# Kernel tuning notes

Measured on AMD Instinct MI355X. Metric: run time of the kernel, lower is better.

The kernel has to match this reference:

```python
import jax, jax.numpy as jnp
import numpy as np

EPS = 1e-5
NHEAD = 8
NEG = -1e9  # matches -inf masked-fill semantics; rows never fully masked after fallback


def layer_norm(x, g, b):
    m = jnp.mean(x, axis=-1, keepdims=True)
    v = jnp.var(x, axis=-1, keepdims=True)
    return (x - m) * jax.lax.rsqrt(v + EPS) * g + b


def mha(q, k, v, Wqkv, bqkv, Wo, bo, bias=None):
    # torch nn.MultiheadAttention math (batch_first). Wqkv: [C, 3C] (jax layout).
    B, N, C = q.shape
    M = k.shape[1]
    d = C // NHEAD
    Wq, Wk, Wv = jnp.split(Wqkv, 3, axis=1)
    bq, bk, bv = jnp.split(bqkv, 3)
    qp = (q @ Wq + bq).reshape(B, N, NHEAD, d)
    kp = (k @ Wk + bk).reshape(B, M, NHEAD, d)
    vp = (v @ Wv + bv).reshape(B, M, NHEAD, d)
    s = jnp.einsum('bnhd,bmhd->bhnm', qp, kp) / np.sqrt(d).astype(q.dtype)
    if bias is not None:
        s = s + bias  # [B,1,N,M] broadcast over heads
    a = jax.nn.softmax(s, axis=-1)
    o = jnp.einsum('bhnm,bmhd->bnhd', a, vp).reshape(B, N, C)
    return o @ Wo + bo


def setup_inputs() -> dict:
    key = jax.random.key(0)
    B, Nq, HW, C, F = 8, 100, 4096, 512, 2048
    ks = jax.random.split(key, 16)
    s = 0.02
    inp = {
        'q': jax.random.normal(ks[0], (B, Nq, C), jnp.float32),
        'kv': jax.random.normal(ks[1], (B, HW, C), jnp.float32),
        'mask_bin': jax.random.randint(ks[2], (B, Nq, HW), 0, 2, jnp.int32),
        # MaskedXAttn: attn params + norm_q/norm_kv
        'xa_Wqkv': jax.random.normal(ks[3], (C, 3 * C), jnp.float32) * s,
        'xa_bqkv': jnp.zeros((3 * C,), jnp.float32),
        'xa_Wo': jax.random.normal(ks[4], (C, C), jnp.float32) * s,
        'xa_bo': jnp.zeros((C,), jnp.float32),
        'xa_gq': jnp.ones((C,), jnp.float32),
        'xa_bq_ln': jnp.zeros((C,), jnp.float32),
        'xa_gkv': jnp.ones((C,), jnp.float32),
        'xa_bkv_ln': jnp.zeros((C,), jnp.float32),
        # self-attention
        'sa_Wqkv': jax.random.normal(ks[5], (C, 3 * C), jnp.float32) * s,
        'sa_bqkv': jnp.zeros((3 * C,), jnp.float32),
        'sa_Wo': jax.random.normal(ks[6], (C, C), jnp.float32) * s,
        'sa_bo': jnp.zeros((C,), jnp.float32),
        # norms
        'n1_g': jnp.ones((C,), jnp.float32), 'n1_b': jnp.zeros((C,), jnp.float32),
        'n2_g': jnp.ones((C,), jnp.float32), 'n2_b': jnp.zeros((C,), jnp.float32),
        # FFN (MLP with num_layers=2: Linear(C,F), ReLU, Linear(F,C))
        'ff_W1': jax.random.normal(ks[7], (C, F), jnp.float32) * s,
        'ff_b1': jnp.zeros((F,), jnp.float32),
        'ff_W2': jax.random.normal(ks[8], (F, C), jnp.float32) * s,
        'ff_b2': jnp.zeros((C,), jnp.float32),
    }
    return inp


def reference(q, kv, mask_bin,
              xa_Wqkv, xa_bqkv, xa_Wo, xa_bo, xa_gq, xa_bq_ln, xa_gkv, xa_bkv_ln,
              sa_Wqkv, sa_bqkv, sa_Wo, sa_bo,
              n1_g, n1_b, n2_g, n2_b,
              ff_W1, ff_b1, ff_W2, ff_b2):
    # --- masked cross-attention (vectorized equivalent of per-query loop) ---
    qn = layer_norm(q, xa_gq, xa_bq_ln)
    kvn = layer_norm(kv, xa_gkv, xa_bkv_ln)
    allow = mask_bin.astype(bool)                      # [B,Nq,HW] True = attend
    row_any = jnp.any(allow, axis=-1, keepdims=True)   # queries with empty mask -> full attention
    eff = jnp.where(row_any, allow, True)
    bias = jnp.where(eff, 0.0, NEG).astype(q.dtype)[:, None, :, :]  # [B,1,Nq,HW]
    xa = mha(qn, kvn, kvn, xa_Wqkv, xa_bqkv, xa_Wo, xa_bo, bias=bias)
    q = q + xa
    # --- self-attention over queries ---
    qn1 = layer_norm(q, n1_g, n1_b)
    sa = mha(qn1, qn1, qn1, sa_Wqkv, sa_bqkv, sa_Wo, sa_bo)
    q = q + sa
    # --- FFN ---
    qn2 = layer_norm(q, n2_g, n2_b)
    h = jax.nn.relu(qn2 @ ff_W1 + ff_b1)
    q = q + (h @ ff_W2 + ff_b2)
    return q
```

## Files before the change

### kernel.cpp

```cpp
#include <hip/hip_runtime.h>

typedef unsigned short u16;
typedef unsigned int u32;
typedef __bf16 bf16x8 __attribute__((ext_vector_type(8)));
typedef short s16x4 __attribute__((ext_vector_type(4)));
typedef float f32x4 __attribute__((ext_vector_type(4)));

#define NEG_INF -3.0e38f
#define QSCALE 0.18033688011f

__device__ __forceinline__ u16 f2bf(float f){
  union { float f; u32 u; } v; v.f = f;
  u32 r = v.u + 0x7fffu + ((v.u >> 16) & 1u);
  return (u16)(r >> 16);
}
__device__ __forceinline__ float bf2f(u16 h){
  union { u32 u; float f; } v; v.u = ((u32)h) << 16; return v.f;
}
__device__ __forceinline__ short f2bf_s(float f){
  union { __bf16 h; short s; } cv; cv.h = (__bf16)f; return cv.s;
}

__device__ __forceinline__ f32x4 mfma16(s16x4 a, s16x4 b, f32x4 c){
#if __has_builtin(__builtin_amdgcn_mfma_f32_16x16x16bf16_1k)
  return __builtin_amdgcn_mfma_f32_16x16x16bf16_1k(a, b, c, 0, 0, 0);
#else
  asm("v_mfma_f32_16x16x16_bf16 %0, %1, %2, %0" : "+v"(c) : "v"(a), "v"(b));
  return c;
#endif
}

__device__ __forceinline__ void gl_lds16(const void* g, void* l){
  __builtin_amdgcn_global_load_lds((const __attribute__((address_space(1))) void*)g,
      (__attribute__((address_space(3))) void*)l, 16, 0, 0);
}

__device__ __forceinline__ void ln_body(const float* __restrict__ xr,
    const float* __restrict__ g, const float* __restrict__ b,
    u16* __restrict__ orow, int lane){
  float4 v0 = *(const float4*)(xr + lane * 4);
  float4 v1 = *(const float4*)(xr + 256 + lane * 4);
  float s = v0.x+v0.y+v0.z+v0.w + v1.x+v1.y+v1.z+v1.w;
  float q = v0.x*v0.x+v0.y*v0.y+v0.z*v0.z+v0.w*v0.w
          + v1.x*v1.x+v1.y*v1.y+v1.z*v1.z+v1.w*v1.w;
  #pragma unroll
  for (int d=1; d<64; d<<=1){ s += __shfl_xor(s, d, 64); q += __shfl_xor(q, d, 64); }
  float mean = s * (1.0f/512.0f);
  float var  = q * (1.0f/512.0f) - mean*mean;
  float rs = rsqrtf(var + 1e-5f);
  float4 g0 = *(const float4*)(g + lane*4), g1 = *(const float4*)(g + 256 + lane*4);
  float4 b0 = *(const float4*)(b + lane*4), b1 = *(const float4*)(b + 256 + lane*4);
  uint2 pa, pb;
  pa.x = (u32)f2bf((v0.x-mean)*rs*g0.x + b0.x) | ((u32)f2bf((v0.y-mean)*rs*g0.y + b0.y) << 16);
  pa.y = (u32)f2bf((v0.z-mean)*rs*g0.z + b0.z) | ((u32)f2bf((v0.w-mean)*rs*g0.w + b0.w) << 16);
  pb.x = (u32)f2bf((v1.x-mean)*rs*g1.x + b1.x) | ((u32)f2bf((v1.y-mean)*rs*g1.y + b1.y) << 16);
  pb.y = (u32)f2bf((v1.z-mean)*rs*g1.z + b1.z) | ((u32)f2bf((v1.w-mean)*rs*g1.w + b1.w) << 16);
  *(uint2*)(orow + lane*4) = pa;
  *(uint2*)(orow + 256 + lane*4) = pb;
}

__global__ __launch_bounds__(256) void ln_rows(const float* __restrict__ x,
    const float* __restrict__ g, const float* __restrict__ b,
    u16* __restrict__ out, int rows){
  int wid = threadIdx.x >> 6, lane = threadIdx.x & 63;
  int row = blockIdx.x * 4 + wid;
  if (row >= rows) return;
  ln_body(x + (size_t)row*512, g, b, out + (size_t)row*512, lane);
}

struct WtJobs {
  const float* W[7]; u16* Wt[7];
  int K[7], Nfull[7], ncol0[7], nt[7], blk0[7];
};
struct PrepArgs {
  WtJobs wt; int totW;
  const float *x0, *g0, *b0; u16* o0; int nb0, rows0;
  const float *x1, *g1, *b1; u16* o1; int nb1, rows1;
};

__global__ __launch_bounds__(256) void prep_all(PrepArgs P){
  __shared__ float tile[32][33];
  int bb = blockIdx.x;
  int tid = threadIdx.x;
  int wid = tid >> 6, lane = tid & 63;
  if (bb < P.totW){
    const WtJobs& J = P.wt;
    const float* W = J.W[0]; u16* Wt = J.Wt[0];
    int K = J.K[0], Nfull = J.Nfull[0], ncol0 = J.ncol0[0], nt = J.nt[0], blk0 = 0;
    #pragma unroll
    for (int i=1;i<7;i++)
      if (bb >= J.blk0[i]){
        W=J.W[i]; Wt=J.Wt[i]; K=J.K[i]; Nfull=J.Nfull[i]; ncol0=J.ncol0[i]; nt=J.nt[i]; blk0=J.blk0[i];
      }
    int lb = bb - blk0;
    int tk = lb / nt, tn = lb % nt;
    int col = tid & 31, kr = tid >> 5;
    #pragma unroll
    for (int i=0;i<4;i++){
      int k = tk*32 + kr + i*8;
      tile[kr + i*8][col] = W[(size_t)k*Nfull + ncol0 + tn*32 + col];
    }
    __syncthreads();
    int nl = tid >> 3, kc = (tid & 7) * 4;
    uint2 o;
    o.x = (u32)f2bf(tile[kc+0][nl]) | ((u32)f2bf(tile[kc+1][nl]) << 16);
    o.y = (u32)f2bf(tile[kc+2][nl]) | ((u32)f2bf(tile[kc+3][nl]) << 16);
    *(uint2*)(Wt + (size_t)(tn*32 + nl)*K + tk*32 + kc) = o;
  } else if (bb < P.totW + P.nb0){
    int row = (bb - P.totW)*4 + wid;
    if (row >= P.rows0) return;
    ln_body(P.x0 + (size_t)row*512, P.g0, P.b0, P.o0 + (size_t)row*512, lane);
  } else {
    int row = (bb - P.totW - P.nb0)*4 + wid;
    if (row >= P.rows1) return;
    ln_body(P.x1 + (size_t)row*512, P.g1, P.b1, P.o1 + (size_t)row*512, lane);
  }
}

struct GemmJob {
  const u16* A; const u16* Bt; const float* bias;
  float* outf; u16* outb; const float* res; u16* out2;
  int M, N, K, lda, k0, ksplit, scale_cols, T1, rows_per_b, vstride, swz, brmap, blk0, nblk;
};
struct GemmJobs {
  GemmJob j[2]; int njobs;
  const int* mask; u32* mw; int maskBlk0;
};

template<int EPI>
__device__ __forceinline__ void epi_store(const GemmJob& J, f32x4 (&acc)[4][4],
    int m0, int n0, int wm, int wn, int lg, int l15, int ksp, u16* smem){
  if (EPI == 3){
    float bv[4];
    #pragma unroll
    for (int ni=0;ni<4;ni++) bv[ni] = J.bias[n0 + wn*64 + ni*16 + l15];
    if (n0 + 128 <= J.T1){
      #pragma unroll
      for (int ni=0;ni<4;ni++){
        int c = n0 + wn*64 + ni*16 + l15;
        #pragma unroll
        for (int mi=0;mi<4;mi++){
          int mr0 = m0 + wm*64 + mi*16 + lg*4;
          #pragma unroll
          for (int r4=0;r4<4;r4++)
            J.outb[(size_t)(mr0+r4)*J.T1 + c] = f2bf(acc[mi][ni][r4] + bv[ni]);
        }
      }
    } else {
      __syncthreads();
      char* scr = (char*)(smem + (wm*2 + wn)*4096);
      #pragma unroll
      for (int ni=0;ni<4;ni++){
        int f_loc = ni*16 + l15;
        #pragma unroll
        for (int mi=0;mi<4;mi++){
          int kb = mi*32 + lg*8;
          uint2 o;
          o.x = (u32)f2bf(acc[mi][ni][0]+bv[ni]) | ((u32)f2bf(acc[mi][ni][1]+bv[ni])<<16);
          o.y = (u32)f2bf(acc[mi][ni][2]+bv[ni]) | ((u32)f2bf(acc[mi][ni][3]+bv[ni])<<16);
          *(uint2*)(scr + f_loc*128 + (kb ^ ((f_loc&7)<<4))) = o;
        }
      }
      int lane = lg*16 + l15;
      int m_base = m0 + wm*64;
      int bidx = m_base >> 12;
      int key0 = m_base & 4095;
      int kc = lane & 7;
      #pragma unroll
      for (int it=0; it<8; it++){
        int f_loc = it*8 + (lane >> 3);
        uint4 v = *(const uint4*)(scr + f_loc*128 + ((kc<<4) ^ ((f_loc&7)<<4)));
        int fg = (n0 - J.T1) + wn*64 + f_loc;
        *(uint4*)(J.out2 + ((size_t)bidx*512 + fg)*(size_t)J.vstride + key0 + kc*8) = v;
      }
    }
  } else if (EPI == 4){
    #pragma unroll
    for (int mi=0;mi<4;mi++){
      #pragma unroll
      for (int r4=0;r4<4;r4++){
        int m = m0 + wm*64 + mi*16 + lg*4 + r4;
        if (m >= J.M) continue;
        float rb = J.bias[m];
        #pragma unroll
        for (int ni=0;ni<4;ni++){
          int c = n0 + wn*64 + ni*16 + l15;
          J.outb[(size_t)m*J.N + c] = f2bf(acc[mi][ni][r4] + rb);
        }
      }
    }
  } else if (EPI == 5){
    float* po_ = J.outf + (size_t)ksp*J.M*J.N;
    #pragma unroll
    for (int mi=0;mi<4;mi++){
      #pragma unroll
      for (int r4=0;r4<4;r4++){
        int m = m0 + wm*64 + mi*16 + lg*4 + r4;
        if (m >= J.M) continue;
        #pragma unroll
        for (int ni=0;ni<4;ni++){
          int c = n0 + wn*64 + ni*16 + l15;
          po_[(size_t)m*J.N + c] = acc[mi][ni][r4];
        }
      }
    }
  } else {
    float bv[4], scl[4];
    #pragma unroll
    for (int ni=0;ni<4;ni++){
      int c = n0 + wn*64 + ni*16 + l15;
      bv[ni]  = J.bias[c];
      scl[ni] = (c < J.scale_cols) ? QSCALE : 1.0f;
    }
    #pragma unroll
    for (int mi=0;mi<4;mi++){
      #pragma unroll
      for (int r4=0;r4<4;r4++){
        int m = m0 + wm*64 + mi*16 + lg*4 + r4;
        if (m >= J.M) continue;
        #pragma unroll
        for (int ni=0;ni<4;ni++){
          int c = n0 + wn*64 + ni*16 + l15;
          float v = acc[mi][ni][r4] + bv[ni];
          if (EPI == 0){
            J.outb[(size_t)m*J.N + c] = f2bf(v*scl[ni]);
          } else if (EPI == 1){
            J.outb[(size_t)m*J.N + c] = f2bf(fmaxf(v, 0.0f));
          } else {
            J.outf[(size_t)m*J.N + c] = v + J.res[(size_t)m*J.N + c];
          }
        }
      }
    }
  }
}

template<int EPI>
__device__ __forceinline__ void gemm_block(const GemmJob& J, int bidIn, u16* smem){
  u16* As = smem;
  u16* Bs = smem + 8192;
  int bid = bidIn;
  int ksp = 0;
  if (J.ksplit > 1){ ksp = bid / J.nblk; bid = bid % J.nblk; }
  if (J.swz){ int cpx = J.nblk >> 3; bid = (bid & 7)*cpx + (bid >> 3); }
  int NT = J.N >> 7;
  int mt = bid / NT, nt = bid % NT;
  int m0 = mt << 7, n0 = nt << 7;
  int kofs = J.k0 + ksp * J.K;
  int tid = threadIdx.x;
  int wid = tid >> 6, lane = tid & 63;
  int wm = wid >> 1, wn = wid & 1;
  int lg = lane >> 4, l15 = lane & 15;

  f32x4 acc[4][4] = {};
  int ktiles = J.K >> 6;
  for (int kt = 0; kt < ktiles; ++kt){
    int k0 = kofs + (kt << 6);
    if (kt) __syncthreads();
    #pragma unroll
    for (int i=0;i<4;i++){
      int L = i*4096 + tid*16;
      int T = L ^ (((L>>7)&7)<<4);
      int row = T >> 7, colb = T & 127;
      int ga = m0 + row; if (ga > J.M-1) ga = J.M-1;
      gl_lds16((const char*)J.A + ((size_t)ga*J.lda + k0)*2 + colb, (char*)As + L);
    }
    #pragma unroll
    for (int i=0;i<4;i++){
      int L = i*4096 + tid*16;
      int T = L ^ (((L>>7)&7)<<4);
      int row = T >> 7, colb = T & 127;
      int rowg = n0 + row;
      if (J.brmap){ int rb = rowg & 127; rowg = (rowg>>7)*J.brmap + (rb < J.brmap ? rb : J.brmap-1); }
      gl_lds16((const char*)J.Bt + ((size_t)rowg*J.lda + k0)*2 + colb, (char*)Bs + L);
    }
    __syncthreads();
    #pragma unroll
    for (int ks=0; ks<2; ++ks){
      bf16x8 af[4], bfr[4];
      #pragma unroll
      for (int mi=0; mi<4; ++mi){
        int r = wm*64 + mi*16 + l15;
        int byt = r*128 + ks*64 + lg*16;
        af[mi] = *(const bf16x8*)((const char*)As + (byt ^ ((r&7)<<4)));
      }
      #pragma unroll
      for (int ni=0; ni<4; ++ni){
        int r = wn*64 + ni*16 + l15;
        int byt = r*128 + ks*64 + lg*16;
        bfr[ni] = *(const bf16x8*)((const char*)Bs + (byt ^ ((r&7)<<4)));
      }
      __builtin_amdgcn_s_setprio(1);
      #pragma unroll
      for (int mi=0;mi<4;mi++)
        #pragma unroll
        for (int ni=0;ni<4;ni++)
          acc[mi][ni] = __builtin_amdgcn_mfma_f32_16x16x32_bf16(af[mi], bfr[ni], acc[mi][ni], 0,0,0);
      __builtin_amdgcn_s_setprio(0);
    }
  }
  epi_store<EPI>(J, acc, m0, n0, wm, wn, lg, l15, ksp, smem);
}

template<int EPIA, int EPIB>
__global__ __launch_bounds__(256) void gemm_multi(GemmJobs G){
  __shared__ __align__(16) u16 smem[16384];
  if (G.mask && (int)blockIdx.x >= G.maskBlk0){
    unsigned long long* blds = (unsigned long long*)smem;
    int tid = threadIdx.x;
    int wid = tid >> 6;
    int lb = (int)blockIdx.x - G.maskBlk0;
    int r0 = lb*2 + (wid >> 1);
    int word = tid & 127;
    const int* mr = G.mask + (size_t)r0*4096 + word*32;
    u32 w = 0;
    #pragma unroll
    for (int j=0;j<32;j+=4){
      int4 v = *(const int4*)(mr + j);
      w |= (u32)(v.x!=0) << j;
      w |= (u32)(v.y!=0) << (j+1);
      w |= (u32)(v.z!=0) << (j+2);
      w |= (u32)(v.w!=0) << (j+3);
    }
    blds[wid] = __ballot(w != 0);
    __syncthreads();
    bool any = (wid < 2) ? ((blds[0] | blds[1]) != 0ull) : ((blds[2] | blds[3]) != 0ull);
    G.mw[(size_t)r0*128 + word] = any ? w : 0xffffffffu;
    return;
  }
  bool second = (G.njobs > 1) && ((int)blockIdx.x >= G.j[1].blk0);
  if (second) gemm_block<EPIB>(G.j[1], (int)blockIdx.x - G.j[1].blk0, smem);
  else        gemm_block<EPIA>(G.j[0], (int)blockIdx.x, smem);
}

__global__ __launch_bounds__(256) void splitk_reduce(
    const float* __restrict__ part, int nsplit, const float* __restrict__ bias,
    const float* __restrict__ res, float* __restrict__ out, int N, int total4)
{
  int idx = (blockIdx.x*256 + threadIdx.x);
  if (idx >= total4) return;
  int e0 = idx*4;
  size_t MN = (size_t)total4*4;
  float4 a = *(const float4*)(part + e0);
  #pragma unroll
  for (int s=1;s<4;s++){
    float4 p = *(const float4*)(part + s*MN + e0);
    a.x += p.x; a.y += p.y; a.z += p.z; a.w += p.w;
  }
  float4 r = *(const float4*)(res + e0);
  int c = e0 & (N-1);
  float4 bv = *(const float4*)(bias + c);
  float4 o;
  o.x = a.x + r.x + bv.x; o.y = a.y + r.y + bv.y;
  o.z = a.z + r.z + bv.z; o.w = a.w + r.w + bv.w;
  *(float4*)(out + e0) = o;
}

template<bool PARTIAL, bool HASMASK, int NTILES>
__global__ __launch_bounds__(256) void attn_kernel(
    const u16* __restrict__ Qp, int ldq,
    const u16* __restrict__ Kp, int ldk, int kcol0,
    const u16* __restrict__ VT, size_t vbs, int vfs,
    const u32* __restrict__ maskw,
    float* __restrict__ pm, float* __restrict__ pl, u16* __restrict__ po,
    u16* __restrict__ o_out,
    int nq, int mk, int S, int H, int Bp, int swz)
{
  __shared__ __align__(16) u16 Ks[2*4096];
  __shared__ __align__(16) u16 Vs[2*4096];
  int bid = blockIdx.x;
  if (swz){ int cpx = gridDim.x >> 3; bid = (bid & 7)*cpx + (bid >> 3); }
  int s = bid % S; int h = (bid / S) % H; int b = bid / (S*H);
  int tid = threadIdx.x, wid = tid>>6, lane = tid&63;
  int lg = lane>>4, l15 = lane&15;
  int qbase = b*nq;
  int kps = mk / S;
  int kbeg = s * kps;
  int mwld = mk >> 5;
  int krel = lg*4;

  bf16x8 qf[2][2];
  #pragma unroll
  for (int mt=0;mt<2;mt++){
    int qr = wid*32 + mt*16 + l15; int qc = qr < nq ? qr : nq-1;
    #pragma unroll
    for (int ks=0;ks<2;ks++)
      qf[mt][ks] = *(const bf16x8*)(Qp + (size_t)(qbase+qc)*ldq + h*64 + ks*32 + lg*8);
  }
  u32 wmw[2][2*NTILES];
  if (HASMASK){
    #pragma unroll
    for (int mt=0;mt<2;mt++){
      int qc = (wid*32 + mt*16 + l15) < nq ? (wid*32 + mt*16 + l15) : nq-1;
      const u32* mrow = maskw + (size_t)(qbase+qc)*mwld + (kbeg>>5);
      #pragma unroll
      for (int wi=0; wi<2*NTILES; wi+=4){
        uint4 v = *(const uint4*)(mrow + wi);
        wmw[mt][wi+0]=v.x; wmw[mt][wi+1]=v.y; wmw[mt][wi+2]=v.z; wmw[mt][wi+3]=v.w;
      }
    }
  }

  float m_r[2] = {NEG_INF, NEG_INF};
  float l_r[2] = {0.0f, 0.0f};
  f32x4 of[2][4] = {};

  auto stage = [&](int t_, int bufi){
    int kb_ = kbeg + t_*64;
    #pragma unroll
    for (int i=0;i<2;i++){
      int idx = i*256 + tid;
      int key = idx>>3, sd = idx&7;
      int kc = kb_ + key; if (kc > mk-1) kc = mk-1;
      const char* src = (const char*)(Kp + (size_t)(b*mk + kc)*ldk + kcol0 + h*64) + ((sd ^ (key&7))<<4);
      gl_lds16(src, (char*)Ks + bufi*8192 + idx*16);
    }
    #pragma unroll
    for (int i=0;i<2;i++){
      int idx = i*256 + tid;
      int f = idx>>3, sd = idx&7;
      const char* src = (const char*)(VT + (size_t)b*vbs + (size_t)(h*64+f)*vfs + kb_) + ((sd ^ (f&7))<<4);
      gl_lds16(src, (char*)Vs + bufi*8192 + idx*16);
    }
  };

  stage(0, 0);

  #pragma unroll
  for (int t=0;t<NTILES;t++){
    if (t+1 < NTILES){
      stage(t+1, (t+1)&1);
      asm volatile("s_waitcnt vmcnt(4)" ::: "memory");
    } else {
      asm volatile("s_waitcnt vmcnt(0)" ::: "memory");
    }
    __builtin_amdgcn_s_barrier();

    const char* Kb = (const char*)Ks + (t&1)*8192;
    const char* Vb = (const char*)Vs + (t&1)*8192;
    int kb = kbeg + t*64;

    f32x4 sT[4][2] = {};
    #pragma unroll
    for (int nt2=0;nt2<4;nt2++){
      bf16x8 k0 = *(const bf16x8*)(Kb + ((nt2*16+l15)<<7) + (((lg  ) ^ (l15&7))<<4));
      bf16x8 k1 = *(const bf16x8*)(Kb + ((nt2*16+l15)<<7) + (((4+lg) ^ (l15&7))<<4));
      __builtin_amdgcn_s_setprio(1);
      #pragma unroll
      for (int mt=0;mt<2;mt++){
        sT[nt2][mt] = __builtin_amdgcn_mfma_f32_16x16x32_bf16(k0, qf[mt][0], sT[nt2][mt], 0,0,0);
        sT[nt2][mt] = __builtin_amdgcn_mfma_f32_16x16x32_bf16(k1, qf[mt][1], sT[nt2][mt], 0,0,0);
      }
      __builtin_amdgcn_s_setprio(0);
    }

    s16x4 pb[2][4];
    #pragma unroll
    for (int mt=0;mt<2;mt++){
      float mx = NEG_INF;
      #pragma unroll
      for (int nt2=0;nt2<4;nt2++){
        u32 wb = 0;
        if (HASMASK) wb = wmw[mt][t*2 + (nt2>>1)] >> (((nt2&1)<<4) + krel);
        #pragma unroll
        for (int r=0;r<4;r++){
          bool ok = HASMASK ? (((wb>>r)&1u) != 0) : (kb + nt2*16 + krel + r < mk);
          float sv = ok ? sT[nt2][mt][r] : NEG_INF;
          sT[nt2][mt][r] = sv;
          mx = fmaxf(mx, sv);
        }
      }
      mx = fmaxf(mx, __shfl_xor(mx, 16, 64));
      mx = fmaxf(mx, __shfl_xor(mx, 32, 64));
      if (!__all(mx <= m_r[mt] + 8.0f)){
        float mnew = fmaxf(m_r[mt], mx);
        float corr = exp2f(m_r[mt] - mnew);
        m_r[mt] = mnew;
        l_r[mt] *= corr;
        #pragma unroll
        for (int nf=0;nf<4;nf++) of[mt][nf] *= corr;
      }
      float ps = 0.0f;
      #pragma unroll
      for (int nt2=0;nt2<4;nt2++)
        #pragma unroll
        for (int r=0;r<4;r++){
          float p = exp2f(sT[nt2][mt][r] - m_r[mt]);
          ps += p;
          pb[mt][nt2][r] = f2bf_s(p);
        }
      ps += __shfl_xor(ps, 16, 64);
      ps += __shfl_xor(ps, 32, 64);
      l_r[mt] += ps;
    }

    #pragma unroll
    for (int nf=0;nf<4;nf++){
      s16x4 vf[4];
      #pragma unroll
      for (int nt2=0;nt2<4;nt2++){
        int slot = (nt2*2 + (lg>>1)) ^ (l15&7);
        vf[nt2] = *(const s16x4*)(Vb + ((nf*16+l15)<<7) + (slot<<4) + ((lg&1)<<3));
      }
      __builtin_amdgcn_s_setprio(1);
      #pragma unroll
      for (int mt=0;mt<2;mt++)
        #pragma unroll
        for (int nt2=0;nt2<4;nt2++)
          of[mt][nf] = mfma16(vf[nt2], pb[mt][nt2], of[mt][nf]);
      __builtin_amdgcn_s_setprio(0);
    }
    __builtin_amdgcn_s_barrier();
  }

  #pragma unroll
  for (int mt=0;mt<2;mt++){
    int q = wid*32 + mt*16 + l15;
    if (q < nq){
      if (PARTIAL){
        size_t base = (((size_t)(s*Bp + b)*H + h)*128 + q);
        if (lg == 0){ pm[base] = m_r[mt]; pl[base] = l_r[mt]; }
        #pragma unroll
        for (int nf=0;nf<4;nf++){
          uint2 o;
          o.x = (u32)f2bf(of[mt][nf][0]) | ((u32)f2bf(of[mt][nf][1])<<16);
          o.y = (u32)f2bf(of[mt][nf][2]) | ((u32)f2bf(of[mt][nf][3])<<16);
          *(uint2*)(po + base*64 + nf*16 + lg*4) = o;
        }
      } else {
        float inv = 1.0f / l_r[mt];
        #pragma unroll
        for (int nf=0;nf<4;nf++){
          uint2 o;
          o.x = (u32)f2bf(of[mt][nf][0]*inv) | ((u32)f2bf(of[mt][nf][1]*inv)<<16);
          o.y = (u32)f2bf(of[mt][nf][2]*inv) | ((u32)f2bf(of[mt][nf][3]*inv)<<16);
          *(uint2*)(o_out + (size_t)(qbase+q)*512 + h*64 + nf*16 + lg*4) = o;
        }
      }
    }
  }
}

__global__ __launch_bounds__(64) void attn_combine(
    const float* __restrict__ pm, const float* __restrict__ pl, const u16* __restrict__ po,
    u16* __restrict__ o_out, int S, int Bp, int H, int nq)
{
  int bid = blockIdx.x;
  int q = bid % nq; int h = (bid / nq) % H; int b = bid / (nq*H);
  int f = threadIdx.x;
  float mstar = NEG_INF;
  for (int s=0;s<S;s++){
    size_t idx = (((size_t)(s*Bp + b)*H + h)*128 + q);
    mstar = fmaxf(mstar, pm[idx]);
  }
  float L = 0.0f, acc = 0.0f;
  for (int s=0;s<S;s++){
    size_t idx = (((size_t)(s*Bp + b)*H + h)*128 + q);
    float w = exp2f(pm[idx] - mstar);
    L += w * pl[idx];
    acc += w * bf2f(po[idx*64 + f]);
  }
  o_out[((size_t)b*nq + q)*512 + h*64 + f] = f2bf(acc / L);
}

extern "C" void kernel_launch(void* const* d_in, const int* in_sizes, int n_in,
                              void* d_out, int out_size, void* d_ws, size_t ws_size,
                              hipStream_t stream){
  const float* q_in    = (const float*)d_in[0];
  const float* kv_in   = (const float*)d_in[1];
  const int*   maskb   = (const int*)d_in[2];
  const float* xa_Wqkv = (const float*)d_in[3];
  const float* xa_bqkv = (const float*)d_in[4];
  const float* xa_Wo   = (const float*)d_in[5];
  const float* xa_bo   = (const float*)d_in[6];
  const float* xa_gq   = (const float*)d_in[7];
  const float* xa_bq   = (const float*)d_in[8];
  const float* xa_gkv  = (const float*)d_in[9];
  const float* xa_bkv  = (const float*)d_in[10];
  const float* sa_Wqkv = (const float*)d_in[11];
  const float* sa_bqkv = (const float*)d_in[12];
  const float* sa_Wo   = (const float*)d_in[13];
  const float* sa_bo   = (const float*)d_in[14];
  const float* n1_g = (const float*)d_in[15];
  const float* n1_b = (const float*)d_in[16];
  const float* n2_g = (const float*)d_in[17];
  const float* n2_b = (const float*)d_in[18];
  const float* ff_W1 = (const float*)d_in[19];
  const float* ff_b1 = (const float*)d_in[20];
  const float* ff_W2 = (const float*)d_in[21];
  const float* ff_b2 = (const float*)d_in[22];

  char* ws = (char*)d_ws;
  size_t off = 0;
  auto alloc = [&](size_t bytes)->char*{ char* p = ws + off; off = (off + bytes + 255) & ~(size_t)255; return p; };
  u16* wq  = (u16*)alloc((size_t)512*512*2);
  u16* wkv = (u16*)alloc((size_t)1024*512*2);
  u16* wsa = (u16*)alloc((size_t)1536*512*2);
  u16* wxo = (u16*)alloc((size_t)512*512*2);
  u16* wso = (u16*)alloc((size_t)512*512*2);
  u16* wf1 = (u16*)alloc((size_t)2048*512*2);
  u16* wf2 = (u16*)alloc((size_t)512*2048*2);
  u16* qn  = (u16*)alloc((size_t)800*512*2);
  u16* qp  = (u16*)alloc((size_t)800*512*2);
  u32* mw  = (u32*)alloc((size_t)800*128*4);
  u16* kp  = (u16*)alloc((size_t)32768*512*2);
  u16* vpT = (u16*)alloc((size_t)8*512*4096*2);
  size_t reuse_off = off;
  u16* kvn = (u16*)alloc((size_t)32768*512*2);
  size_t offB = reuse_off;
  auto allocB = [&](size_t bytes)->char*{ char* p = ws + offB; offB = (offB + bytes + 255) & ~(size_t)255; return p; };
  const int S = 16;
  float* pm   = (float*)allocB((size_t)S*64*128*4);
  float* pl   = (float*)allocB((size_t)S*64*128*4);
  u16*   po   = (u16*)allocB((size_t)S*64*128*64*2);
  u16* o_xa   = (u16*)allocB((size_t)800*512*2);
  float* x1   = (float*)allocB((size_t)800*512*4);
  u16* qn1    = (u16*)allocB((size_t)800*512*2);
  u16* saqkv  = (u16*)allocB((size_t)800*1024*2);
  u16* vT2sa  = (u16*)allocB((size_t)512*1024*2);
  u16* o_sa   = (u16*)allocB((size_t)800*512*2);
  float* x2   = (float*)allocB((size_t)800*512*4);
  u16* qn2    = (u16*)allocB((size_t)800*512*2);
  u16* hbuf   = (u16*)allocB((size_t)800*2048*2);
  float* fpart = pm;

  PrepArgs P;
  P.wt.W[0]=xa_Wqkv; P.wt.Wt[0]=wq;  P.wt.K[0]=512;  P.wt.Nfull[0]=1536; P.wt.ncol0[0]=0;   P.wt.nt[0]=16;
  P.wt.W[1]=xa_Wqkv; P.wt.Wt[1]=wkv; P.wt.K[1]=512;  P.wt.Nfull[1]=1536; P.wt.ncol0[1]=512; P.wt.nt[1]=32;
  P.wt.W[2]=sa_Wqkv; P.wt.Wt[2]=wsa; P.wt.K[2]=512;  P.wt.Nfull[2]=1536; P.wt.ncol0[2]=0;   P.wt.nt[2]=48;
  P.wt.W[3]=xa_Wo;   P.wt.Wt[3]=wxo; P.wt.K[3]=512;  P.wt.Nfull[3]=512;  P.wt.ncol0[3]=0;   P.wt.nt[3]=16;
  P.wt.W[4]=sa_Wo;   P.wt.Wt[4]=wso; P.wt.K[4]=512;  P.wt.Nfull[4]=512;  P.wt.ncol0[4]=0;   P.wt.nt[4]=16;
  P.wt.W[5]=ff_W1;   P.wt.Wt[5]=wf1; P.wt.K[5]=512;  P.wt.Nfull[5]=2048; P.wt.ncol0[5]=0;   P.wt.nt[5]=64;
  P.wt.W[6]=ff_W2;   P.wt.Wt[6]=wf2; P.wt.K[6]=2048; P.wt.Nfull[6]=512;  P.wt.ncol0[6]=0;   P.wt.nt[6]=16;
  int tot = 0;
  for (int i=0;i<7;i++){ P.wt.blk0[i] = tot; tot += (P.wt.K[i]/32)*P.wt.nt[i]; }
  P.totW = tot;
  P.x0=q_in;  P.g0=xa_gq;  P.b0=xa_bq;  P.o0=qn;  P.nb0=200;  P.rows0=800;
  P.x1=kv_in; P.g1=xa_gkv; P.b1=xa_bkv; P.o1=kvn; P.nb1=8192; P.rows1=32768;
  prep_all<<<tot + 200 + 8192, 256, 0, stream>>>(P);

  auto mkjob = [&](const u16*A, const u16*Bt, const float*bias, float*outf, u16*outb,
                   const float*res, u16*out2, int M, int N, int K, int lda, int k0,
                   int ksplit, int sc, int T1, int rpb, int vst, int swz, int brm,
                   int blk0, int nblk)->GemmJob{
    GemmJob j; j.A=A; j.Bt=Bt; j.bias=bias; j.outf=outf; j.outb=outb; j.res=res; j.out2=out2;
    j.M=M; j.N=N; j.K=K; j.lda=lda; j.k0=k0; j.ksplit=ksplit; j.scale_cols=sc; j.T1=T1;
    j.rows_per_b=rpb; j.vstride=vst; j.swz=swz; j.brmap=brm; j.blk0=blk0; j.nblk=nblk;
    return j;
  };

  {
    GemmJobs g;
    g.j[0] = mkjob(qn, wq, xa_bqkv, nullptr, qp, nullptr, nullptr,
                   800, 512, 512, 512, 0, 1, 512, 0,1,1, 0,0, 0, 28);
    g.j[1] = mkjob(kvn, wkv, xa_bqkv+512, nullptr, kp, nullptr, vpT,
                   32768, 1024, 512, 512, 0, 1, 0, 512, 4096, 4096, 1, 0, 28, 2048);
    g.njobs = 2;
    g.mask = maskb; g.mw = mw; g.maskBlk0 = 28 + 2048;
    gemm_multi<0,3><<<28 + 2048 + 400, 256, 0, stream>>>(g);
  }
  attn_kernel<true,true,4><<<8*8*S, 256, 0, stream>>>(
      qp, 512, kp, 512, 0, vpT, (size_t)512*4096, 4096, mw,
      pm, pl, po, nullptr, 100, 4096, S, 8, 8, 1);
  attn_combine<<<8*8*100, 64, 0, stream>>>(pm, pl, po, o_xa, S, 8, 8, 100);
  {
    GemmJobs g;
    g.j[0] = mkjob(o_xa, wxo, xa_bo, x1, nullptr, q_in, nullptr,
                   800, 512, 512, 512, 0, 1, 0, 0,1,1, 0,0, 0, 28);
    g.j[1] = g.j[0]; g.njobs = 1;
    g.mask = nullptr; g.mw = nullptr; g.maskBlk0 = 1<<30;
    gemm_multi<2,2><<<28, 256, 0, stream>>>(g);
  }
  ln_rows<<<200, 256, 0, stream>>>(x1, n1_g, n1_b, qn1, 800);
  {
    GemmJobs g;
    g.j[0] = mkjob(qn1, wsa, sa_bqkv, nullptr, saqkv, nullptr, nullptr,
                   800, 1024, 512, 512, 0, 1, 512, 0,1,1, 0,0, 0, 56);
    g.j[1] = mkjob(wsa + (size_t)1024*512, qn1, sa_bqkv+1024, nullptr, vT2sa, nullptr, nullptr,
                   512, 1024, 512, 512, 0, 1, 0, 0,1,1, 0, 100, 56, 32);
    g.njobs = 2;
    g.mask = nullptr; g.mw = nullptr; g.maskBlk0 = 1<<30;
    gemm_multi<0,4><<<56 + 32, 256, 0, stream>>>(g);
  }
  attn_kernel<false,false,2><<<64, 256, 0, stream>>>(
      saqkv, 1024, saqkv, 1024, 512, vT2sa, (size_t)128, 1024, nullptr,
      nullptr, nullptr, nullptr, o_sa, 100, 100, 1, 8, 8, 0);
  {
    GemmJobs g;
    g.j[0] = mkjob(o_sa, wso, sa_bo, x2, nullptr, x1, nullptr,
                   800, 512, 512, 512, 0, 1, 0, 0,1,1, 0,0, 0, 28);
    g.j[1] = g.j[0]; g.njobs = 1;
    g.mask = nullptr; g.mw = nullptr; g.maskBlk0 = 1<<30;
    gemm_multi<2,2><<<28, 256, 0, stream>>>(g);
  }
  ln_rows<<<200, 256, 0, stream>>>(x2, n2_g, n2_b, qn2, 800);
  {
    GemmJobs g;
    g.j[0] = mkjob(qn2, wf1, ff_b1, nullptr, hbuf, nullptr, nullptr,
                   800, 2048, 512, 512, 0, 1, 0, 0,1,1, 0,0, 0, 112);
    g.j[1] = g.j[0]; g.njobs = 1;
    g.mask = nullptr; g.mw = nullptr; g.maskBlk0 = 1<<30;
    gemm_multi<1,1><<<112, 256, 0, stream>>>(g);
  }
  {
    GemmJobs g;
    g.j[0] = mkjob(hbuf, wf2, nullptr, fpart, nullptr, nullptr, nullptr,
                   800, 512, 512, 2048, 0, 4, 0, 0,1,1, 0,0, 0, 28);
    g.j[1] = g.j[0]; g.njobs = 1;
    g.mask = nullptr; g.mw = nullptr; g.maskBlk0 = 1<<30;
    gemm_multi<5,5><<<112, 256, 0, stream>>>(g);
  }
  splitk_reduce<<<(800*512/4 + 255)/256, 256, 0, stream>>>(
      fpart, 4, ff_b2, x2, (float*)d_out, 512, 800*512/4);
}
```

Baseline: 220.5 us.

## Fuse split-K reduce and attention combine into last-arriving blocks via atomic counters

Removes the separate splitk_reduce and attn_combine kernel launches. Each split block now increments a per-tile (or per batch-head) atomic counter after writing its partial results, and the last block to arrive performs the reduction with bias and residual, or the softmax-merge combine. This saves two launches and their global round trips, at the cost of thread fences, a memset of the counters, and serialized tail work done by a single block per tile.

```diff
diff --git a/kernel.cpp b/kernel.cpp
--- a/kernel.cpp
+++ b/kernel.cpp
@@ -120,6 +120,7 @@
 struct GemmJob {
   const u16* A; const u16* Bt; const float* bias;
   float* outf; u16* outb; const float* res; u16* out2;
+  float* fout; u32* cnt;
   int M, N, K, lda, k0, ksplit, scale_cols, T1, rows_per_b, vstride, swz, brmap, blk0, nblk;
 };
 struct GemmJobs {
@@ -129,7 +130,7 @@
 
 template<int EPI>
 __device__ __forceinline__ void epi_store(const GemmJob& J, f32x4 (&acc)[4][4],
-    int m0, int n0, int wm, int wn, int lg, int l15, int ksp, u16* smem){
+    int m0, int n0, int wm, int wn, int lg, int l15, int ksp, int tileBid, u16* smem){
   if (EPI == 3){
     float bv[4];
     #pragma unroll
@@ -201,6 +202,33 @@
         for (int ni=0;ni<4;ni++){
           int c = n0 + wn*64 + ni*16 + l15;
           po_[(size_t)m*J.N + c] = acc[mi][ni][r4];
+        }
+      }
+    }
+    volatile u32* flag = (u32*)smem;
+    __threadfence();
+    __syncthreads();
+    if (threadIdx.x == 0) flag[0] = atomicAdd(&J.cnt[tileBid], 1u);
+    __syncthreads();
+    if (flag[0] == 3u){
+      __threadfence();
+      for (int e = threadIdx.x; e < 128*32; e += 256){
+        int r = e >> 5, c4 = (e & 31) * 4;
+        int m = m0 + r;
+        if (m < J.M){
+          size_t off0 = (size_t)m*J.N + n0 + c4;
+          float4 a = *(const float4*)(J.outf + off0);
+          #pragma unroll
+          for (int s2=1; s2<4; s2++){
+            float4 p = *(const float4*)(J.outf + (size_t)s2*J.M*J.N + off0);
+            a.x+=p.x; a.y+=p.y; a.z+=p.z; a.w+=p.w;
+          }
+          float4 rr = *(const float4*)(J.res + off0);
+          float4 bv4 = *(const float4*)(J.bias + n0 + c4);
+          float4 o;
+          o.x=a.x+rr.x+bv4.x; o.y=a.y+rr.y+bv4.y;
+          o.z=a.z+rr.z+bv4.z; o.w=a.w+rr.w+bv4.w;
+          *(float4*)(J.fout + off0) = o;
         }
       }
     }
@@ -243,6 +271,7 @@
   int ksp = 0;
   if (J.ksplit > 1){ ksp = bid / J.nblk; bid = bid % J.nblk; }
   if (J.swz){ int cpx = J.nblk >> 3; bid = (bid & 7)*cpx + (bid >> 3); }
+  int tileBid = bid;
   int NT = J.N >> 7;
   int mt = bid / NT, nt = bid % NT;
   int m0 = mt << 7, n0 = nt << 7;
@@ -299,7 +328,7 @@
       __builtin_amdgcn_s_setprio(0);
     }
   }
-  epi_store<EPI>(J, acc, m0, n0, wm, wn, lg, l15, ksp, smem);
+  epi_store<EPI>(J, acc, m0, n0, wm, wn, lg, l15, ksp, tileBid, smem);
 }
 
 template<int EPIA, int EPIB>
@@ -333,29 +362,6 @@
   else        gemm_block<EPIA>(G.j[0], (int)blockIdx.x, smem);
 }
 
-__global__ __launch_bounds__(256) void splitk_reduce(
-    const float* __restrict__ part, int nsplit, const float* __restrict__ bias,
-    const float* __restrict__ res, float* __restrict__ out, int N, int total4)
-{
-  int idx = (blockIdx.x*256 + threadIdx.x);
-  if (idx >= total4) return;
-  int e0 = idx*4;
-  size_t MN = (size_t)total4*4;
-  float4 a = *(const float4*)(part + e0);
-  #pragma unroll
-  for (int s=1;s<4;s++){
-    float4 p = *(const float4*)(part + s*MN + e0);
-    a.x += p.x; a.y += p.y; a.z += p.z; a.w += p.w;
-  }
-  float4 r = *(const float4*)(res + e0);
-  int c = e0 & (N-1);
-  float4 bv = *(const float4*)(bias + c);
-  float4 o;
-  o.x = a.x + r.x + bv.x; o.y = a.y + r.y + bv.y;
-  o.z = a.z + r.z + bv.z; o.w = a.w + r.w + bv.w;
-  *(float4*)(out + e0) = o;
-}
-
 template<bool PARTIAL, bool HASMASK, int NTILES>
 __global__ __launch_bounds__(256) void attn_kernel(
     const u16* __restrict__ Qp, int ldq,
@@ -363,11 +369,12 @@
     const u16* __restrict__ VT, size_t vbs, int vfs,
     const u32* __restrict__ maskw,
     float* __restrict__ pm, float* __restrict__ pl, u16* __restrict__ po,
-    u16* __restrict__ o_out,
+    u16* __restrict__ o_out, u32* __restrict__ cnt,
     int nq, int mk, int S, int H, int Bp, int swz)
 {
   __shared__ __align__(16) u16 Ks[2*4096];
   __shared__ __align__(16) u16 Vs[2*4096];
+  __shared__ u32 lastArr;
   int bid = blockIdx.x;
   if (swz){ int cpx = gridDim.x >> 3; bid = (bid & 7)*cpx + (bid >> 3); }
   int s = bid % S; int h = (bid / S) % H; int b = bid / (S*H);
@@ -539,28 +546,32 @@
       }
     }
   }
-}
-
-__global__ __launch_bounds__(64) void attn_combine(
-    const float* __restrict__ pm, const float* __restrict__ pl, const u16* __restrict__ po,
-    u16* __restrict__ o_out, int S, int Bp, int H, int nq)
-{
-  int bid = blockIdx.x;
-  int q = bid % nq; int h = (bid / nq) % H; int b = bid / (nq*H);
-  int f = threadIdx.x;
-  float mstar = NEG_INF;
-  for (int s=0;s<S;s++){
-    size_t idx = (((size_t)(s*Bp + b)*H + h)*128 + q);
-    mstar = fmaxf(mstar, pm[idx]);
-  }
-  float L = 0.0f, acc = 0.0f;
-  for (int s=0;s<S;s++){
-    size_t idx = (((size_t)(s*Bp + b)*H + h)*128 + q);
-    float w = exp2f(pm[idx] - mstar);
-    L += w * pl[idx];
-    acc += w * bf2f(po[idx*64 + f]);
-  }
-  o_out[((size_t)b*nq + q)*512 + h*64 + f] = f2bf(acc / L);
+
+  if (PARTIAL){
+    __threadfence();
+    __syncthreads();
+    if (tid == 0) lastArr = atomicAdd(&cnt[b*H + h], 1u);
+    __syncthreads();
+    if (lastArr == (u32)(S-1)){
+      __threadfence();
+      int f = lane;
+      for (int q = wid; q < nq; q += 4){
+        float mstar = NEG_INF;
+        for (int s2=0; s2<S; s2++){
+          size_t idx = (((size_t)(s2*Bp + b)*H + h)*128 + q);
+          mstar = fmaxf(mstar, pm[idx]);
+        }
+        float L = 0.0f, acc = 0.0f;
+        for (int s2=0; s2<S; s2++){
+          size_t idx = (((size_t)(s2*Bp + b)*H + h)*128 + q);
+          float w = exp2f(pm[idx] - mstar);
+          L += w * pl[idx];
+          acc += w * bf2f(po[idx*64 + f]);
+        }
+        o_out[((size_t)b*nq + q)*512 + h*64 + f] = f2bf(acc / L);
+      }
+    }
+  }
 }
 
 extern "C" void kernel_launch(void* const* d_in, const int* in_sizes, int n_in,
@@ -603,6 +614,7 @@
   u16* qn  = (u16*)alloc((size_t)800*512*2);
   u16* qp  = (u16*)alloc((size_t)800*512*2);
   u32* mw  = (u32*)alloc((size_t)800*128*4);
+  u32* cnt = (u32*)alloc(512);
   u16* kp  = (u16*)alloc((size_t)32768*512*2);
   u16* vpT = (u16*)alloc((size_t)8*512*4096*2);
   size_t reuse_off = off;
@@ -638,12 +650,14 @@
   P.x0=q_in;  P.g0=xa_gq;  P.b0=xa_bq;  P.o0=qn;  P.nb0=200;  P.rows0=800;
   P.x1=kv_in; P.g1=xa_gkv; P.b1=xa_bkv; P.o1=kvn; P.nb1=8192; P.rows1=32768;
   prep_all<<<tot + 200 + 8192, 256, 0, stream>>>(P);
+  hipMemsetAsync(cnt, 0, 512, stream);
 
   auto mkjob = [&](const u16*A, const u16*Bt, const float*bias, float*outf, u16*outb,
                    const float*res, u16*out2, int M, int N, int K, int lda, int k0,
                    int ksplit, int sc, int T1, int rpb, int vst, int swz, int brm,
                    int blk0, int nblk)->GemmJob{
     GemmJob j; j.A=A; j.Bt=Bt; j.bias=bias; j.outf=outf; j.outb=outb; j.res=res; j.out2=out2;
+    j.fout=nullptr; j.cnt=nullptr;
     j.M=M; j.N=N; j.K=K; j.lda=lda; j.k0=k0; j.ksplit=ksplit; j.scale_cols=sc; j.T1=T1;
     j.rows_per_b=rpb; j.vstride=vst; j.swz=swz; j.brmap=brm; j.blk0=blk0; j.nblk=nblk;
     return j;
@@ -661,8 +675,7 @@
   }
   attn_kernel<true,true,4><<<8*8*S, 256, 0, stream>>>(
       qp, 512, kp, 512, 0, vpT, (size_t)512*4096, 4096, mw,
-      pm, pl, po, nullptr, 100, 4096, S, 8, 8, 1);
-  attn_combine<<<8*8*100, 64, 0, stream>>>(pm, pl, po, o_xa, S, 8, 8, 100);
+      pm, pl, po, o_xa, cnt, 100, 4096, S, 8, 8, 1);
   {
     GemmJobs g;
     g.j[0] = mkjob(o_xa, wxo, xa_bo, x1, nullptr, q_in, nullptr,
@@ -684,7 +697,7 @@
   }
   attn_kernel<false,false,2><<<64, 256, 0, stream>>>(
       saqkv, 1024, saqkv, 1024, 512, vT2sa, (size_t)128, 1024, nullptr,
-      nullptr, nullptr, nullptr, o_sa, 100, 100, 1, 8, 8, 0);
+      nullptr, nullptr, nullptr, o_sa, nullptr, 100, 100, 1, 8, 8, 0);
   {
     GemmJobs g;
     g.j[0] = mkjob(o_sa, wso, sa_bo, x2, nullptr, x1, nullptr,
@@ -704,12 +717,12 @@
   }
   {
     GemmJobs g;
-    g.j[0] = mkjob(hbuf, wf2, nullptr, fpart, nullptr, nullptr, nullptr,
+    g.j[0] = mkjob(hbuf, wf2, ff_b2, fpart, nullptr, x2, nullptr,
                    800, 512, 512, 2048, 0, 4, 0, 0,1,1, 0,0, 0, 28);
+    g.j[0].fout = (float*)d_out;
+    g.j[0].cnt  = cnt + 64;
     g.j[1] = g.j[0]; g.njobs = 1;
     g.mask = nullptr; g.mw = nullptr; g.maskBlk0 = 1<<30;
     gemm_multi<5,5><<<112, 256, 0, stream>>>(g);
   }
-  splitk_reduce<<<(800*512/4 + 255)/256, 256, 0, stream>>>(
-      fpart, 4, ff_b2, x2, (float*)d_out, 512, 800*512/4);
-}
+}
```

New measurement: 555.0 us. 152% more time.
